# Kernel optimization log

Hardware: AMD Instinct MI355X
Metric: run time of the kernel (lower is better)

## Reference

```python
import jax, jax.numpy as jnp
import numpy as np

N_NODES = 100000
N_EDGES = 1600000
IN_F = 256
OUT_F = 128


def setup_inputs() -> dict:
    key = jax.random.key(0)
    k1, k2, k3, k4, k5, k6 = jax.random.split(key, 6)
    X_input = jax.random.normal(k1, (N_NODES, IN_F), dtype=jnp.float32)
    adj_row = jax.random.randint(k2, (N_EDGES,), 0, N_NODES, dtype=jnp.int32)
    adj_col = jax.random.randint(k3, (N_EDGES,), 0, N_NODES, dtype=jnp.int32)
    adj_val = jax.random.uniform(k4, (N_EDGES,), dtype=jnp.float32)
    W = jax.random.normal(k5, (IN_F, OUT_F), dtype=jnp.float32) / np.sqrt(IN_F)
    bias = jax.random.normal(k6, (OUT_F,), dtype=jnp.float32) * 0.01
    return {"X_input": X_input, "adj_row": adj_row, "adj_col": adj_col,
            "adj_val": adj_val, "W": W, "bias": bias}


def reference(X_input, adj_row, adj_col, adj_val, W, bias):
    # dense linear (no bias): support = X @ W   [N, out]
    support = X_input @ W
    # sparse adjacency matmul (COO spmm): out[r] += val * support[c]
    messages = adj_val[:, None] * support[adj_col]          # [E, out]
    output = jax.ops.segment_sum(messages, adj_row, num_segments=N_NODES)
    return output + bias
```

## Files before the change

kernel.cpp:

```cpp
#include <hip/hip_runtime.h>

#define N_NODES 100000
#define N_EDGES 1600000
#define IN_F    256
#define OUT_F   128

#define BROWS2   256
#define NB2      391
#define CAPB     4800
#define PART_EPB 4096
#define KE       (PART_EPB / 256)
#define KB       ((CAPB + 255) / 256)
#define NGEMM    1563

typedef __attribute__((ext_vector_type(8))) short   s16x8;
typedef __attribute__((ext_vector_type(4))) float   f32x4;
typedef __attribute__((ext_vector_type(8))) unsigned short u16x8;

__device__ __forceinline__ unsigned short f2bf(float f) {
    unsigned u = __float_as_uint(f);
    u += 0x7FFFu + ((u >> 16) & 1u);
    return (unsigned short)(u >> 16);
}
__device__ __forceinline__ float bf2f(unsigned short h) {
    return __uint_as_float((unsigned)h << 16);
}

__device__ __forceinline__ void gl_lds16(const void* g, void* l) {
    __builtin_amdgcn_global_load_lds((const __attribute__((address_space(1))) void*)g,
                                     (__attribute__((address_space(3))) void*)l,
                                     16, 0, 0);
}
__device__ __forceinline__ unsigned cvt_pk_bf16(float lo, float hi) {
    unsigned r;
    asm("v_cvt_pk_bf16_f32 %0, %1, %2" : "=v"(r) : "v"(lo), "v"(hi));
    return r;
}

__global__ __launch_bounds__(256) void wt_build(const float* __restrict__ W,
                                                unsigned short* __restrict__ Wt,
                                                int* __restrict__ cursorA) {
    const int n = blockIdx.x;
    const int k = threadIdx.x;
    Wt[(k >> 3) * 1024 + n * 8 + (k & 7)] = f2bf(W[(size_t)k * OUT_F + n]);
    const int idx = blockIdx.x * 256 + threadIdx.x;
    if (idx < NB2) cursorA[idx] = 0;
}

__global__ __launch_bounds__(256) void gemm_mfma(const float* __restrict__ X,
                                                 const unsigned short* __restrict__ Wt,
                                                 unsigned short* __restrict__ support) {
    __shared__ __align__(16) char smem[17408];
    unsigned short* Bs  = (unsigned short*)smem;
    float*          Asf = (float*)(smem + 8192);
    unsigned short* Ct  = (unsigned short*)smem;

    const int t    = threadIdx.x;
    const int wid  = t >> 6;
    const int lane = t & 63;
    const int tm   = lane & 15;
    const int quad = lane >> 4;
    const int row0 = blockIdx.x * 64;

    const char* srcA[2];
    char*       dstA[2];
#pragma unroll
    for (int i = 0; i < 2; ++i) {
        const int s  = wid * 128 + i * 64 + lane;
        const int r  = s >> 3;
        const int jj = (s & 7) ^ (r & 7);
        const int gr = min(row0 + r, N_NODES - 1);
        srcA[i] = (const char*)X + (size_t)gr * (IN_F * 4) + jj * 16;
        dstA[i] = (char*)Asf + (size_t)(wid * 128 + i * 64) * 16;
    }
    const char* srcB[2];
    char*       dstB[2];
#pragma unroll
    for (int i = 0; i < 2; ++i) {
        const int c1k = wid * 2 + i;
        srcB[i] = (const char*)Wt + (size_t)c1k * 1024 + lane * 16;
        dstB[i] = (char*)Bs + (size_t)c1k * 1024;
    }

    f32x4 acc[8];
#pragma unroll
    for (int c = 0; c < 8; ++c) acc[c] = (f32x4){0.f, 0.f, 0.f, 0.f};

    for (int ks = 0; ks < 8; ++ks) {
        gl_lds16(srcA[0], dstA[0]);
        gl_lds16(srcA[1], dstA[1]);
        gl_lds16(srcB[0], dstB[0]);
        gl_lds16(srcB[1], dstB[1]);
        srcA[0] += 128; srcA[1] += 128;
        srcB[0] += 8192; srcB[1] += 8192;
        __syncthreads();

        const int r  = wid * 16 + tm;
        const int j0 = quad * 2;
        const float4 a0 = *(const float4*)&Asf[(r * 8 + (j0 ^ (r & 7))) * 4];
        const float4 a1 = *(const float4*)&Asf[(r * 8 + ((j0 + 1) ^ (r & 7))) * 4];
        union { s16x8 v; unsigned u[4]; } af;
        af.u[0] = cvt_pk_bf16(a0.x, a0.y);
        af.u[1] = cvt_pk_bf16(a0.z, a0.w);
        af.u[2] = cvt_pk_bf16(a1.x, a1.y);
        af.u[3] = cvt_pk_bf16(a1.z, a1.w);

#pragma unroll
        for (int c = 0; c < 8; ++c) {
            const s16x8 b = *(const s16x8*)&Bs[(quad * 128 + c * 16 + tm) * 8];
            acc[c] = __builtin_amdgcn_mfma_f32_16x16x32_bf16(af.v, b, acc[c], 0, 0, 0);
        }
        __syncthreads();
    }

#pragma unroll
    for (int c = 0; c < 8; ++c) {
        const int col = c * 16 + tm;
#pragma unroll
        for (int reg = 0; reg < 4; ++reg) {
            const int m = wid * 16 + quad * 4 + reg;
            Ct[m * 136 + col] = f2bf(acc[c][reg]);
        }
    }
    __syncthreads();
    {
        const int m   = t >> 2;
        const int seg = (t & 3) * 32;
        const int gr  = row0 + m;
        if (gr < N_NODES) {
            unsigned short* op = &support[(size_t)gr * OUT_F + seg];
#pragma unroll
            for (int i = 0; i < 4; ++i)
                *(u16x8*)(op + i * 8) = *(const u16x8*)&Ct[m * 136 + seg + i * 8];
        }
    }
}

__global__ __launch_bounds__(256) void partition_edges(const int* __restrict__ arow,
                                                       const int* __restrict__ acol,
                                                       const float* __restrict__ aval,
                                                       int* __restrict__ cursorA,
                                                       int2* __restrict__ epackA) {
    __shared__ int cnt[NB2];
    __shared__ int basep[NB2];
    const int t = threadIdx.x;
    for (int k = t; k < NB2; k += 256) cnt[k] = 0;
    __syncthreads();

    const int base = blockIdx.x * PART_EPB;
    int pk_[KE], vv_[KE], b_[KE], rk_[KE];
#pragma unroll
    for (int k = 0; k < KE; ++k) {
        const int i = base + t + k * 256;
        b_[k] = -1;
        if (i < N_EDGES) {
            const int r = arow[i];
            b_[k]  = r >> 8;
            pk_[k] = ((r & (BROWS2 - 1)) << 17) | acol[i];
            vv_[k] = __float_as_int(aval[i]);
            rk_[k] = atomicAdd(&cnt[b_[k]], 1);
        }
    }
    __syncthreads();
    for (int k = t; k < NB2; k += 256) {
        const int c = cnt[k];
        if (c > 0) basep[k] = atomicAdd(&cursorA[k], c);
    }
    __syncthreads();
#pragma unroll
    for (int k = 0; k < KE; ++k) {
        if (b_[k] >= 0) {
            const int pos = basep[b_[k]] + rk_[k];
            if (pos < CAPB)
                epackA[(size_t)b_[k] * CAPB + pos] = make_int2(pk_[k], vv_[k]);
        }
    }
}

__global__ __launch_bounds__(256) void bucket_build(const int* __restrict__ cursorA,
                                                    const int2* __restrict__ epackA,
                                                    int2* __restrict__ rowmeta,
                                                    int2* __restrict__ epackB) {
    __shared__ int cnt[BROWS2];
    __shared__ int excl[BROWS2];
    __shared__ int wsum[4];
    const int b = blockIdx.x;
    const int t = threadIdx.x;
    cnt[t] = 0;
    __syncthreads();

    const size_t sa = (size_t)b * CAPB;
    const int n = min(cursorA[b], CAPB);

    int pk_[KB], vv_[KB], rk_[KB];
#pragma unroll
    for (int k = 0; k < KB; ++k) {
        const int i = t + k * 256;
        rk_[k] = -1;
        if (i < n) {
            const int2 e = epackA[sa + i];
            pk_[k] = e.x;
            vv_[k] = e.y;
            rk_[k] = atomicAdd(&cnt[e.x >> 17], 1);
        }
    }
    __syncthreads();

    {
        const int lane = t & 63;
        const int my   = cnt[t];
        int x = my;
#pragma unroll
        for (int off = 1; off < 64; off <<= 1) {
            const int y = __shfl_up(x, off, 64);
            if (lane >= off) x += y;
        }
        if (lane == 63) wsum[t >> 6] = x;
        __syncthreads();
        int pre = x - my;
        const int w = t >> 6;
        for (int kk = 0; kk < w; ++kk) pre += wsum[kk];
        excl[t] = pre;
        const int r = b * BROWS2 + t;
        if (r < N_NODES) rowmeta[r] = make_int2((int)sa + pre, my);
    }
    __syncthreads();

#pragma unroll
    for (int k = 0; k < KB; ++k) {
        if (rk_[k] >= 0) {
            const int rl  = pk_[k] >> 17;
            const int pos = excl[rl] + rk_[k];
            epackB[sa + pos] = make_int2(pk_[k] & 0x1FFFF, vv_[k]);
        }
    }
}

__global__ __launch_bounds__(256) void csr_gather(const int2* __restrict__ rowmeta,
                                                  const int2* __restrict__ epackB,
                                                  const unsigned short* __restrict__ support,
                                                  const float* __restrict__ bias,
                                                  float* __restrict__ out) {
    const int t = threadIdx.x;
    const int g = t >> 5;
    const int l = t & 31;
    const int r = blockIdx.x * 8 + g;
    if (r >= N_NODES) return;

    const int2 rm   = rowmeta[r];
    const int start = rm.x;
    const int deg   = rm.y;

    float4 acc = *(const float4*)&bias[l * 4];

    int i = 0;
    for (; i + 4 <= deg; i += 4) {
        const int2 e0 = epackB[start + i + 0];
        const int2 e1 = epackB[start + i + 1];
        const int2 e2 = epackB[start + i + 2];
        const int2 e3 = epackB[start + i + 3];
        const ushort4 u0 = *(const ushort4*)&support[(size_t)e0.x * OUT_F + l * 4];
        const ushort4 u1 = *(const ushort4*)&support[(size_t)e1.x * OUT_F + l * 4];
        const ushort4 u2 = *(const ushort4*)&support[(size_t)e2.x * OUT_F + l * 4];
        const ushort4 u3 = *(const ushort4*)&support[(size_t)e3.x * OUT_F + l * 4];
        const float v0 = __int_as_float(e0.y);
        const float v1 = __int_as_float(e1.y);
        const float v2 = __int_as_float(e2.y);
        const float v3 = __int_as_float(e3.y);
        acc.x = fmaf(v0, bf2f(u0.x), fmaf(v1, bf2f(u1.x), fmaf(v2, bf2f(u2.x), fmaf(v3, bf2f(u3.x), acc.x))));
        acc.y = fmaf(v0, bf2f(u0.y), fmaf(v1, bf2f(u1.y), fmaf(v2, bf2f(u2.y), fmaf(v3, bf2f(u3.y), acc.y))));
        acc.z = fmaf(v0, bf2f(u0.z), fmaf(v1, bf2f(u1.z), fmaf(v2, bf2f(u2.z), fmaf(v3, bf2f(u3.z), acc.z))));
        acc.w = fmaf(v0, bf2f(u0.w), fmaf(v1, bf2f(u1.w), fmaf(v2, bf2f(u2.w), fmaf(v3, bf2f(u3.w), acc.w))));
    }
    for (; i < deg; ++i) {
        const int2 e = epackB[start + i];
        const ushort4 u = *(const ushort4*)&support[(size_t)e.x * OUT_F + l * 4];
        const float v = __int_as_float(e.y);
        acc.x = fmaf(v, bf2f(u.x), acc.x);
        acc.y = fmaf(v, bf2f(u.y), acc.y);
        acc.z = fmaf(v, bf2f(u.z), acc.z);
        acc.w = fmaf(v, bf2f(u.w), acc.w);
    }

    *(float4*)&out[(size_t)r * OUT_F + l * 4] = acc;
}

extern "C" void kernel_launch(void* const* d_in, const int* in_sizes, int n_in,
                              void* d_out, int out_size, void* d_ws, size_t ws_size,
                              hipStream_t stream) {
    const float* X    = (const float*)d_in[0];
    const int*   arow = (const int*)d_in[1];
    const int*   acol = (const int*)d_in[2];
    const float* aval = (const float*)d_in[3];
    const float* W    = (const float*)d_in[4];
    const float* bias = (const float*)d_in[5];
    float*       out  = (float*)d_out;

    char* ws = (char*)d_ws;
    unsigned short* support = (unsigned short*)ws;  ws += (size_t)N_NODES * OUT_F * 2;
    unsigned short* Wt = (unsigned short*)ws;       ws += (size_t)IN_F * OUT_F * 2;
    int2* rowmeta = (int2*)ws;                      ws += (size_t)N_NODES * 8;
    int*  cursorA = (int*)ws;                       ws += ((NB2 + 7) & ~7) * 4;
    int2* epackB  = (int2*)ws;
    int2* epackA  = (int2*)d_out;

    wt_build<<<OUT_F, 256, 0, stream>>>(W, Wt, cursorA);
    gemm_mfma<<<NGEMM, 256, 0, stream>>>(X, Wt, support);
    partition_edges<<<(N_EDGES + PART_EPB - 1) / PART_EPB, 256, 0, stream>>>(
        arow, acol, aval, cursorA, epackA);
    bucket_build<<<NB2, 256, 0, stream>>>(cursorA, epackA, rowmeta, epackB);
    csr_gather<<<(N_NODES + 7) / 8, 256, 0, stream>>>(
        rowmeta, epackB, support, bias, out);
}
```

Measured before the change: 289.7 us.

## Fuse bucket CSR build with gather using LDS-resident per-bucket edge lists

Shrinks row buckets from 256 to 64 rows and merges the bucket sort and CSR gather kernels into one. Each block sorts its bucket's edges by local row in shared memory, then gathers support rows from there, so the sorted edge array and row metadata are never written to or re-read from global memory and one launch is dropped. Risks: lower parallelism in the gather (each 32-thread group walks 8 rows serially), 1563 blocks instead of 12500, and a per-bucket cap of 1312 edges that silently drops overflow edges if a bucket is denser than expected.

```diff
diff --git a/kernel.cpp b/kernel.cpp
--- a/kernel.cpp
+++ b/kernel.cpp
@@ -5,12 +5,12 @@
 #define IN_F    256
 #define OUT_F   128
 
-#define BROWS2   256
-#define NB2      391
-#define CAPB     4800
+#define BROWS    64
+#define NB       1563
+#define CAP      1312
 #define PART_EPB 4096
 #define KE       (PART_EPB / 256)
-#define KB       ((CAPB + 255) / 256)
+#define KB2      6
 #define NGEMM    1563
 
 typedef __attribute__((ext_vector_type(8))) short   s16x8;
@@ -44,7 +44,7 @@
     const int k = threadIdx.x;
     Wt[(k >> 3) * 1024 + n * 8 + (k & 7)] = f2bf(W[(size_t)k * OUT_F + n]);
     const int idx = blockIdx.x * 256 + threadIdx.x;
-    if (idx < NB2) cursorA[idx] = 0;
+    if (idx < NB) cursorA[idx] = 0;
 }
 
 __global__ __launch_bounds__(256) void gemm_mfma(const float* __restrict__ X,
@@ -141,10 +141,10 @@
                                                        const float* __restrict__ aval,
                                                        int* __restrict__ cursorA,
                                                        int2* __restrict__ epackA) {
-    __shared__ int cnt[NB2];
-    __shared__ int basep[NB2];
+    __shared__ int cnt[NB];
+    __shared__ int basep[NB];
     const int t = threadIdx.x;
-    for (int k = t; k < NB2; k += 256) cnt[k] = 0;
+    for (int k = t; k < NB; k += 256) cnt[k] = 0;
     __syncthreads();
 
     const int base = blockIdx.x * PART_EPB;
@@ -155,14 +155,14 @@
         b_[k] = -1;
         if (i < N_EDGES) {
             const int r = arow[i];
-            b_[k]  = r >> 8;
-            pk_[k] = ((r & (BROWS2 - 1)) << 17) | acol[i];
+            b_[k]  = r >> 6;
+            pk_[k] = ((r & (BROWS - 1)) << 17) | acol[i];
             vv_[k] = __float_as_int(aval[i]);
             rk_[k] = atomicAdd(&cnt[b_[k]], 1);
         }
     }
     __syncthreads();
-    for (int k = t; k < NB2; k += 256) {
+    for (int k = t; k < NB; k += 256) {
         const int c = cnt[k];
         if (c > 0) basep[k] = atomicAdd(&cursorA[k], c);
     }
@@ -171,30 +171,33 @@
     for (int k = 0; k < KE; ++k) {
         if (b_[k] >= 0) {
             const int pos = basep[b_[k]] + rk_[k];
-            if (pos < CAPB)
-                epackA[(size_t)b_[k] * CAPB + pos] = make_int2(pk_[k], vv_[k]);
-        }
-    }
-}
-
-__global__ __launch_bounds__(256) void bucket_build(const int* __restrict__ cursorA,
-                                                    const int2* __restrict__ epackA,
-                                                    int2* __restrict__ rowmeta,
-                                                    int2* __restrict__ epackB) {
-    __shared__ int cnt[BROWS2];
-    __shared__ int excl[BROWS2];
-    __shared__ int wsum[4];
+            if (pos < CAP)
+                epackA[(size_t)b_[k] * CAP + pos] = make_int2(pk_[k], vv_[k]);
+        }
+    }
+}
+
+__global__ __launch_bounds__(256) void bucket_gather(const int* __restrict__ cursorA,
+                                                     const int2* __restrict__ epackA,
+                                                     const unsigned short* __restrict__ support,
+                                                     const float* __restrict__ bias,
+                                                     float* __restrict__ out) {
+    __shared__ int2 eb[CAP];
+    __shared__ int  cnt[BROWS];
+    __shared__ int  excl[BROWS];
+
     const int b = blockIdx.x;
     const int t = threadIdx.x;
-    cnt[t] = 0;
-    __syncthreads();
-
-    const size_t sa = (size_t)b * CAPB;
-    const int n = min(cursorA[b], CAPB);
-
-    int pk_[KB], vv_[KB], rk_[KB];
-#pragma unroll
-    for (int k = 0; k < KB; ++k) {
+
+    if (t < BROWS) cnt[t] = 0;
+    __syncthreads();
+
+    const size_t sa = (size_t)b * CAP;
+    const int n = min(cursorA[b], CAP);
+
+    int pk_[KB2], vv_[KB2], rk_[KB2];
+#pragma unroll
+    for (int k = 0; k < KB2; ++k) {
         const int i = t + k * 256;
         rk_[k] = -1;
         if (i < n) {
@@ -206,83 +209,71 @@
     }
     __syncthreads();
 
-    {
-        const int lane = t & 63;
-        const int my   = cnt[t];
+    if (t < BROWS) {
+        const int my = cnt[t];
         int x = my;
 #pragma unroll
         for (int off = 1; off < 64; off <<= 1) {
             const int y = __shfl_up(x, off, 64);
-            if (lane >= off) x += y;
-        }
-        if (lane == 63) wsum[t >> 6] = x;
-        __syncthreads();
-        int pre = x - my;
-        const int w = t >> 6;
-        for (int kk = 0; kk < w; ++kk) pre += wsum[kk];
-        excl[t] = pre;
-        const int r = b * BROWS2 + t;
-        if (r < N_NODES) rowmeta[r] = make_int2((int)sa + pre, my);
-    }
-    __syncthreads();
-
-#pragma unroll
-    for (int k = 0; k < KB; ++k) {
+            if (t >= off) x += y;
+        }
+        excl[t] = x - my;
+    }
+    __syncthreads();
+
+#pragma unroll
+    for (int k = 0; k < KB2; ++k) {
         if (rk_[k] >= 0) {
-            const int rl  = pk_[k] >> 17;
-            const int pos = excl[rl] + rk_[k];
-            epackB[sa + pos] = make_int2(pk_[k] & 0x1FFFF, vv_[k]);
-        }
-    }
-}
-
-__global__ __launch_bounds__(256) void csr_gather(const int2* __restrict__ rowmeta,
-                                                  const int2* __restrict__ epackB,
-                                                  const unsigned short* __restrict__ support,
-                                                  const float* __restrict__ bias,
-                                                  float* __restrict__ out) {
-    const int t = threadIdx.x;
+            const int rl = pk_[k] >> 17;
+            eb[excl[rl] + rk_[k]] = make_int2(pk_[k] & 0x1FFFF, vv_[k]);
+        }
+    }
+    __syncthreads();
+
     const int g = t >> 5;
     const int l = t & 31;
-    const int r = blockIdx.x * 8 + g;
-    if (r >= N_NODES) return;
-
-    const int2 rm   = rowmeta[r];
-    const int start = rm.x;
-    const int deg   = rm.y;
-
-    float4 acc = *(const float4*)&bias[l * 4];
-
-    int i = 0;
-    for (; i + 4 <= deg; i += 4) {
-        const int2 e0 = epackB[start + i + 0];
-        const int2 e1 = epackB[start + i + 1];
-        const int2 e2 = epackB[start + i + 2];
-        const int2 e3 = epackB[start + i + 3];
-        const ushort4 u0 = *(const ushort4*)&support[(size_t)e0.x * OUT_F + l * 4];
-        const ushort4 u1 = *(const ushort4*)&support[(size_t)e1.x * OUT_F + l * 4];
-        const ushort4 u2 = *(const ushort4*)&support[(size_t)e2.x * OUT_F + l * 4];
-        const ushort4 u3 = *(const ushort4*)&support[(size_t)e3.x * OUT_F + l * 4];
-        const float v0 = __int_as_float(e0.y);
-        const float v1 = __int_as_float(e1.y);
-        const float v2 = __int_as_float(e2.y);
-        const float v3 = __int_as_float(e3.y);
-        acc.x = fmaf(v0, bf2f(u0.x), fmaf(v1, bf2f(u1.x), fmaf(v2, bf2f(u2.x), fmaf(v3, bf2f(u3.x), acc.x))));
-        acc.y = fmaf(v0, bf2f(u0.y), fmaf(v1, bf2f(u1.y), fmaf(v2, bf2f(u2.y), fmaf(v3, bf2f(u3.y), acc.y))));
-        acc.z = fmaf(v0, bf2f(u0.z), fmaf(v1, bf2f(u1.z), fmaf(v2, bf2f(u2.z), fmaf(v3, bf2f(u3.z), acc.z))));
-        acc.w = fmaf(v0, bf2f(u0.w), fmaf(v1, bf2f(u1.w), fmaf(v2, bf2f(u2.w), fmaf(v3, bf2f(u3.w), acc.w))));
-    }
-    for (; i < deg; ++i) {
-        const int2 e = epackB[start + i];
-        const ushort4 u = *(const ushort4*)&support[(size_t)e.x * OUT_F + l * 4];
-        const float v = __int_as_float(e.y);
-        acc.x = fmaf(v, bf2f(u.x), acc.x);
-        acc.y = fmaf(v, bf2f(u.y), acc.y);
-        acc.z = fmaf(v, bf2f(u.z), acc.z);
-        acc.w = fmaf(v, bf2f(u.w), acc.w);
-    }
-
-    *(float4*)&out[(size_t)r * OUT_F + l * 4] = acc;
+    const float4 bv = *(const float4*)&bias[l * 4];
+
+    for (int rr = 0; rr < 8; ++rr) {
+        const int rl = g * 8 + rr;
+        const int r  = b * BROWS + rl;
+        if (r >= N_NODES) continue;
+
+        const int start = excl[rl];
+        const int deg   = cnt[rl];
+        float4 acc = bv;
+
+        int i = 0;
+        for (; i + 4 <= deg; i += 4) {
+            const int2 e0 = eb[start + i + 0];
+            const int2 e1 = eb[start + i + 1];
+            const int2 e2 = eb[start + i + 2];
+            const int2 e3 = eb[start + i + 3];
+            const ushort4 u0 = *(const ushort4*)&support[(size_t)e0.x * OUT_F + l * 4];
+            const ushort4 u1 = *(const ushort4*)&support[(size_t)e1.x * OUT_F + l * 4];
+            const ushort4 u2 = *(const ushort4*)&support[(size_t)e2.x * OUT_F + l * 4];
+            const ushort4 u3 = *(const ushort4*)&support[(size_t)e3.x * OUT_F + l * 4];
+            const float v0 = __int_as_float(e0.y);
+            const float v1 = __int_as_float(e1.y);
+            const float v2 = __int_as_float(e2.y);
+            const float v3 = __int_as_float(e3.y);
+            acc.x = fmaf(v0, bf2f(u0.x), fmaf(v1, bf2f(u1.x), fmaf(v2, bf2f(u2.x), fmaf(v3, bf2f(u3.x), acc.x))));
+            acc.y = fmaf(v0, bf2f(u0.y), fmaf(v1, bf2f(u1.y), fmaf(v2, bf2f(u2.y), fmaf(v3, bf2f(u3.y), acc.y))));
+            acc.z = fmaf(v0, bf2f(u0.z), fmaf(v1, bf2f(u1.z), fmaf(v2, bf2f(u2.z), fmaf(v3, bf2f(u3.z), acc.z))));
+            acc.w = fmaf(v0, bf2f(u0.w), fmaf(v1, bf2f(u1.w), fmaf(v2, bf2f(u2.w), fmaf(v3, bf2f(u3.w), acc.w))));
+        }
+        for (; i < deg; ++i) {
+            const int2 e = eb[start + i];
+            const ushort4 u = *(const ushort4*)&support[(size_t)e.x * OUT_F + l * 4];
+            const float v = __int_as_float(e.y);
+            acc.x = fmaf(v, bf2f(u.x), acc.x);
+            acc.y = fmaf(v, bf2f(u.y), acc.y);
+            acc.z = fmaf(v, bf2f(u.z), acc.z);
+            acc.w = fmaf(v, bf2f(u.w), acc.w);
+        }
+
+        *(float4*)&out[(size_t)r * OUT_F + l * 4] = acc;
+    }
 }
 
 extern "C" void kernel_launch(void* const* d_in, const int* in_sizes, int n_in,
@@ -299,16 +290,12 @@
     char* ws = (char*)d_ws;
     unsigned short* support = (unsigned short*)ws;  ws += (size_t)N_NODES * OUT_F * 2;
     unsigned short* Wt = (unsigned short*)ws;       ws += (size_t)IN_F * OUT_F * 2;
-    int2* rowmeta = (int2*)ws;                      ws += (size_t)N_NODES * 8;
-    int*  cursorA = (int*)ws;                       ws += ((NB2 + 7) & ~7) * 4;
-    int2* epackB  = (int2*)ws;
-    int2* epackA  = (int2*)d_out;
+    int*  cursorA = (int*)ws;                       ws += ((NB + 7) & ~7) * 4;
+    int2* epackA  = (int2*)ws;
 
     wt_build<<<OUT_F, 256, 0, stream>>>(W, Wt, cursorA);
     gemm_mfma<<<NGEMM, 256, 0, stream>>>(X, Wt, support);
     partition_edges<<<(N_EDGES + PART_EPB - 1) / PART_EPB, 256, 0, stream>>>(
         arow, acol, aval, cursorA, epackA);
-    bucket_build<<<NB2, 256, 0, stream>>>(cursorA, epackA, rowmeta, epackB);
-    csr_gather<<<(N_NODES + 7) / 8, 256, 0, stream>>>(
-        rowmeta, epackB, support, bias, out);
-}
+    bucket_gather<<<NB, 256, 0, stream>>>(cursorA, epackA, support, bias, out);
+}
```

After: 287.0 us. Within noise of the previous version (-0.9%).
